# Performance work log

Hardware: AMD Instinct MI355X
Metric: run time of the kernel (lower is better)

## Reference

```python
import jax, jax.numpy as jnp
import numpy as np

B, N = 32, 4096
SA1 = (512, 0.2, 32)   # npoint, radius, nsample
SA2 = (128, 0.4, 64)
MLP1 = [3, 64, 64, 128]
MLP2 = [131, 128, 128, 256]   # 128 feats + 3 relative xyz
MLP3 = [259, 256, 512, 1024]  # 256 feats + 3 xyz (group_all)


def _mk_mlp(key, dims, prefix, d):
    for i in range(len(dims) - 1):
        key, k1 = jax.random.split(key)
        d[f"{prefix}_w{i}"] = jax.random.normal(k1, (dims[i], dims[i + 1]), jnp.float32) * (1.0 / np.sqrt(dims[i]))
        d[f"{prefix}_b{i}"] = jnp.zeros((dims[i + 1],), jnp.float32)
    return key


def setup_inputs() -> dict:
    key = jax.random.key(0)
    d = {}
    key, kx = jax.random.split(key)
    d["xyz"] = jax.random.uniform(kx, (B, N, 3), jnp.float32)  # normalized coords in [0,1)
    key = _mk_mlp(key, MLP1, "sa1", d)
    key = _mk_mlp(key, MLP2, "sa2", d)
    key = _mk_mlp(key, MLP3, "sa3", d)
    key, k1, k2 = jax.random.split(key, 3)
    d["cls_w"] = jax.random.normal(k1, (1024, 1), jnp.float32) * 0.03
    d["cls_b"] = jnp.zeros((1,), jnp.float32)
    d["reg_w"] = jax.random.normal(k2, (1024, 4), jnp.float32) * 0.03
    d["reg_b"] = jnp.zeros((4,), jnp.float32)
    return d


def fps(xyz, npoint):
    """Farthest point sampling. xyz: (B,N,3) -> idx (B,npoint) int32."""
    Bb, Nn, _ = xyz.shape

    def step(carry, _):
        dist, farthest = carry  # (B,N), (B,)
        centroid = jnp.take_along_axis(xyz, farthest[:, None, None], axis=1)  # (B,1,3)
        d = jnp.sum((xyz - centroid) ** 2, axis=-1)  # (B,N)
        dist = jnp.minimum(dist, d)
        nxt = jnp.argmax(dist, axis=-1).astype(jnp.int32)
        return (dist, nxt), farthest

    init = (jnp.full((Bb, Nn), 1e10, xyz.dtype), jnp.zeros((Bb,), jnp.int32))
    _, idx = jax.lax.scan(step, init, None, length=npoint)
    return idx.T  # (B,npoint)


def ball_query(radius, nsample, xyz, new_xyz):
    """xyz: (B,N,3), new_xyz: (B,S,3) -> idx (B,S,nsample) int32."""
    Bb, S, _ = new_xyz.shape
    Nn = xyz.shape[1]
    sqr = jnp.sum((new_xyz[:, :, None, :] - xyz[:, None, :, :]) ** 2, axis=-1)  # (B,S,N)
    idx = jnp.broadcast_to(jnp.arange(Nn, dtype=jnp.int32), (Bb, S, Nn))
    idx = jnp.where(sqr > radius * radius, Nn, idx)
    idx = jnp.sort(idx, axis=-1)[:, :, :nsample]
    first = idx[:, :, :1]
    return jnp.where(idx == Nn, first, idx)  # pad out-of-ball slots with first neighbor


def _sa(xyz, feats, npoint, radius, nsample, ws, bs):
    Bb = xyz.shape[0]
    cidx = fps(xyz, npoint)
    new_xyz = xyz[jnp.arange(Bb)[:, None], cidx]  # (B,S,3)
    gidx = ball_query(radius, nsample, xyz, new_xyz)  # (B,S,K)
    b3 = jnp.arange(Bb)[:, None, None]
    g = xyz[b3, gidx] - new_xyz[:, :, None, :]  # (B,S,K,3) relative coords
    if feats is not None:
        g = jnp.concatenate([g, feats[b3, gidx]], axis=-1)
    for w, b in zip(ws, bs):
        g = jax.nn.relu(g @ w + b)
    return new_xyz, jnp.max(g, axis=2)  # (B,S,C_out)


def _sa_all(xyz, feats, ws, bs):
    g = jnp.concatenate([xyz, feats], axis=-1)[:, None]  # (B,1,S,3+C)
    for w, b in zip(ws, bs):
        g = jax.nn.relu(g @ w + b)
    return jnp.max(g, axis=2)[:, 0]  # (B,C_out)


def reference(xyz, sa1_w0, sa1_b0, sa1_w1, sa1_b1, sa1_w2, sa1_b2,
              sa2_w0, sa2_b0, sa2_w1, sa2_b1, sa2_w2, sa2_b2,
              sa3_w0, sa3_b0, sa3_w1, sa3_b1, sa3_w2, sa3_b2,
              cls_w, cls_b, reg_w, reg_b):
    xyz1, f1 = _sa(xyz, None, SA1[0], SA1[1], SA1[2],
                   [sa1_w0, sa1_w1, sa1_w2], [sa1_b0, sa1_b1, sa1_b2])
    xyz2, f2 = _sa(xyz1, f1, SA2[0], SA2[1], SA2[2],
                   [sa2_w0, sa2_w1, sa2_w2], [sa2_b0, sa2_b1, sa2_b2])
    feat = _sa_all(xyz2, f2, [sa3_w0, sa3_w1, sa3_w2], [sa3_b0, sa3_b1, sa3_b2])  # (B,1024)
    return feat @ cls_w + cls_b, feat @ reg_w + reg_b
```

## Files before the change

### kernel.cpp

```cpp
#include <hip/hip_runtime.h>

#define DEVINL __device__ __forceinline__

typedef __attribute__((ext_vector_type(8))) short bf16x8;
typedef __attribute__((ext_vector_type(8))) unsigned short u16x8;
typedef __attribute__((ext_vector_type(4))) float f32x4;

DEVINL unsigned short f2bh(float f){
  unsigned u = __float_as_uint(f);
  return (unsigned short)((u + 0x7FFFu + ((u >> 16) & 1u)) >> 16);
}
DEVINL float bh2f(unsigned short h){ return __uint_as_float(((unsigned)h) << 16); }

DEVINL unsigned long long dpp_max_u64(unsigned long long k) {
#define DPP_STEP(ctrl)                                                        \
  {                                                                           \
    int hi = (int)(k >> 32), lo = (int)(unsigned)k;                           \
    int oh = __builtin_amdgcn_update_dpp(0, hi, ctrl, 0xF, 0xF, 1);           \
    int ol = __builtin_amdgcn_update_dpp(0, lo, ctrl, 0xF, 0xF, 1);           \
    unsigned long long ok =                                                   \
        ((unsigned long long)(unsigned)oh << 32) | (unsigned)ol;              \
    if (ok > k) k = ok;                                                       \
  }
  DPP_STEP(0x111)
  DPP_STEP(0x112)
  DPP_STEP(0x114)
  DPP_STEP(0x118)
  DPP_STEP(0x142)
  DPP_STEP(0x143)
#undef DPP_STEP
  return k;
}

template<int N, int NP, int NT>
DEVINL void fps_body(const float* __restrict__ xyz, float* __restrict__ nxyz,
                     int b, int t) {
  constexpr int PTS = N / NT;
  constexpr int NW = NT / 64;
  __shared__ float xs[N], ys[N], zs[N];
  __shared__ int farr[NP];
  __shared__ unsigned long long sk[2][(NW > 1 ? NW : 1)];
  float px[PTS], py[PTS], pz[PTS], dst[PTS];
  const float* base = xyz + (size_t)b * N * 3;
#pragma unroll
  for (int j = 0; j < PTS; ++j) {
    int i = t + j * NT;
    float x = base[i * 3 + 0], y = base[i * 3 + 1], z = base[i * 3 + 2];
    px[j] = x; py[j] = y; pz[j] = z;
    xs[i] = x; ys[i] = y; zs[i] = z;
    dst[j] = 1e10f;
  }
  if constexpr (NW > 1) __syncthreads();
  int far = 0;
  const int wv = t >> 6, ln = t & 63;
  for (int s = 0; s < NP; ++s) {
    float cx = xs[far], cy = ys[far], cz = zs[far];
    if (t == 0) farr[s] = far;
    float bv = -1.f; int bi = 0;
#pragma unroll
    for (int j = 0; j < PTS; ++j) {
      float dx = __fsub_rn(px[j], cx), dy = __fsub_rn(py[j], cy), dz = __fsub_rn(pz[j], cz);
      float d = __fadd_rn(__fadd_rn(__fmul_rn(dx, dx), __fmul_rn(dy, dy)), __fmul_rn(dz, dz));
      float nd = fminf(dst[j], d);
      dst[j] = nd;
      int i = t + j * NT;
      if (nd > bv) { bv = nd; bi = i; }
    }
    unsigned long long key =
        ((unsigned long long)__float_as_uint(bv) << 32) | (unsigned)(~bi);
    key = dpp_max_u64(key);
    if constexpr (NW == 1) {
      int rl = __builtin_amdgcn_readlane((int)(unsigned)key, 63);
      far = (int)(~(unsigned)rl);
    } else {
      const int p = s & 1;
      if (ln == 63) sk[p][wv] = key;
      __syncthreads();
      unsigned long long m = sk[p][0];
#pragma unroll
      for (int q = 1; q < NW; ++q) {
        unsigned long long qk = sk[p][q];
        if (qk > m) m = qk;
      }
      far = (int)(~(unsigned)m);
    }
  }
  if constexpr (NW > 1) __syncthreads();
  for (int s2 = t; s2 < NP; s2 += NT) {
    int fi = farr[s2];
    float* o = nxyz + ((size_t)b * NP + s2) * 3;
    o[0] = xs[fi]; o[1] = ys[fi]; o[2] = zs[fi];
  }
}

template<int N, int NS>
DEVINL void bq_body(const float* __restrict__ pts, const float* __restrict__ centers,
                    int* __restrict__ gidx, int Q, float r2, int blk, int t) {
  const int wv = t >> 6, ln = t & 63;
  const int g = blk * 4 + wv;
  const int b = g / Q, q = g % Q;
  const float* pb = pts + (size_t)b * N * 3;
  const float* c = centers + ((size_t)b * Q + q) * 3;
  const float cx = c[0], cy = c[1], cz = c[2];
  __shared__ int gbuf[4][NS];
  int taken = 0;
  for (int base = 0; base < N; base += 64) {
    if (taken >= NS) break;
    int i = base + ln;
    float dx = __fsub_rn(pb[i * 3 + 0], cx), dy = __fsub_rn(pb[i * 3 + 1], cy),
          dz = __fsub_rn(pb[i * 3 + 2], cz);
    float d = __fadd_rn(__fadd_rn(__fmul_rn(dx, dx), __fmul_rn(dy, dy)), __fmul_rn(dz, dz));
    bool in = (d <= r2);
    unsigned long long mk = __ballot(in);
    int rank = __popcll(mk & ((1ull << ln) - 1ull));
    int pos = taken + rank;
    if (in && pos < NS) gbuf[wv][pos] = i;
    taken += (int)__popcll(mk);
  }
  int total = taken < NS ? taken : NS;
  int first = gbuf[wv][0];
  int* out = gidx + ((size_t)b * Q + q) * NS;
  for (int j = ln; j < NS; j += 64) out[j] = (j < total) ? gbuf[wv][j] : first;
}

struct WPEnt { const float* W; unsigned short* hi; unsigned short* lo; int K, N, row0, beg, end; };
struct WPTab { WPEnt e[8]; };
DEVINL void wprep_body(const WPTab& tab, int idx) {
#pragma unroll
  for (int i = 0; i < 8; ++i) {
    const WPEnt& E = tab.e[i];
    if (idx >= E.beg && idx < E.end) {
      int local = idx - E.beg;
      int k = local / E.N, n = local - k * E.N;
      float v = E.W[(size_t)(E.row0 + k) * E.N + n];
      unsigned short h = f2bh(v);
      E.hi[(size_t)n * E.K + k] = h;
      E.lo[(size_t)n * E.K + k] = f2bh(v - bh2f(h));
    }
  }
}

__global__ __launch_bounds__(256) void fps1_wprep_kernel(const float* __restrict__ xyz,
                                                         float* __restrict__ nx1, WPTab tab) {
  if (blockIdx.x < 32) { fps_body<4096, 512, 256>(xyz, nx1, blockIdx.x, threadIdx.x); return; }
  wprep_body(tab, (blockIdx.x - 32) * 256 + threadIdx.x);
}

__global__ __launch_bounds__(256) void fps2_bq1_kernel(const float* __restrict__ xyz,
                                                       const float* __restrict__ nx1,
                                                       int* __restrict__ gidx1,
                                                       float* __restrict__ nx2, float r21) {
  if (blockIdx.x < 32) {
    if (threadIdx.x < 64) fps_body<512, 128, 64>(nx1, nx2, blockIdx.x, threadIdx.x);
    return;
  }
  bq_body<4096, 32>(xyz, nx1, gidx1, 512, r21, blockIdx.x - 32, threadIdx.x);
}

template<int K, int N, int CW, int AS, int WS, bool XYZC, int NTH>
DEVINL void do_layer(const unsigned short* __restrict__ Ghi, const unsigned short* __restrict__ Glo,
                     const float* __restrict__ Wxyz,
                     const float* __restrict__ A, unsigned short* __restrict__ Whi,
                     unsigned short* __restrict__ Wlo, const float* __restrict__ sxyz,
                     f32x4* acc, int t) {
  constexpr int KT = K / 32;
  constexpr int NCH = N / CW;
  constexpr int K8 = K / 8;
  constexpr int SI = (CW * K8) / NTH;
  constexpr int CT = CW / 16;
  const int l = t & 63, wv = t >> 6;

  u16x8 rh[SI], rl[SI];
#pragma unroll
  for (int s = 0; s < SI; ++s) {
    int u = t + s * NTH;
    int nn = u / K8, k8 = (u - nn * K8) * 8;
    rh[s] = *reinterpret_cast<const u16x8*>(Ghi + (size_t)nn * K + k8);
    rl[s] = *reinterpret_cast<const u16x8*>(Glo + (size_t)nn * K + k8);
  }

  bf16x8 ahi[KT], alo[KT];
  {
    const int row = wv * 16 + (l & 15);
    const float* ap = A + row * AS + (l >> 4) * 8;
#pragma unroll
    for (int kt = 0; kt < KT; ++kt) {
      float4 v0 = *reinterpret_cast<const float4*>(ap + kt * 32);
      float4 v1 = *reinterpret_cast<const float4*>(ap + kt * 32 + 4);
      float f[8] = {v0.x, v0.y, v0.z, v0.w, v1.x, v1.y, v1.z, v1.w};
      bf16x8 h, lo2;
#pragma unroll
      for (int j = 0; j < 8; ++j) {
        unsigned short hb = f2bh(f[j]);
        h[j] = (short)hb;
        lo2[j] = (short)f2bh(f[j] - bh2f(hb));
      }
      ahi[kt] = h; alo[kt] = lo2;
    }
  }
#pragma unroll
  for (int i = 0; i < N / 16; ++i) acc[i] = f32x4{0.f, 0.f, 0.f, 0.f};

#pragma unroll
  for (int c = 0; c < NCH; ++c) {
    __syncthreads();
#pragma unroll
    for (int s = 0; s < SI; ++s) {
      int u = t + s * NTH;
      int nn = u / K8, k8 = (u - nn * K8) * 8;
      *reinterpret_cast<u16x8*>(Whi + nn * WS + k8) = rh[s];
      *reinterpret_cast<u16x8*>(Wlo + nn * WS + k8) = rl[s];
    }
    if (c + 1 < NCH) {
#pragma unroll
      for (int s = 0; s < SI; ++s) {
        int u = t + s * NTH;
        int nn = u / K8, k8 = (u - nn * K8) * 8;
        rh[s] = *reinterpret_cast<const u16x8*>(Ghi + (size_t)((c + 1) * CW + nn) * K + k8);
        rl[s] = *reinterpret_cast<const u16x8*>(Glo + (size_t)((c + 1) * CW + nn) * K + k8);
      }
    }
    __syncthreads();
#pragma unroll
    for (int ct = 0; ct < CT; ++ct) {
      const unsigned short* wp = Whi + (ct * 16 + (l & 15)) * WS + (l >> 4) * 8;
      const unsigned short* wq = Wlo + (ct * 16 + (l & 15)) * WS + (l >> 4) * 8;
      f32x4 a = acc[c * CT + ct];
#pragma unroll
      for (int kt = 0; kt < KT; ++kt) {
        bf16x8 wh = *reinterpret_cast<const bf16x8*>(wp + kt * 32);
        bf16x8 wl = *reinterpret_cast<const bf16x8*>(wq + kt * 32);
        a = __builtin_amdgcn_mfma_f32_16x16x32_bf16(ahi[kt], wh, a, 0, 0, 0);
        a = __builtin_amdgcn_mfma_f32_16x16x32_bf16(alo[kt], wh, a, 0, 0, 0);
        a = __builtin_amdgcn_mfma_f32_16x16x32_bf16(ahi[kt], wl, a, 0, 0, 0);
      }
      acc[c * CT + ct] = a;
    }
  }
  if constexpr (XYZC) {
    float xr[4][3];
#pragma unroll
    for (int r = 0; r < 4; ++r) {
      int row = wv * 16 + (l >> 4) * 4 + r;
      xr[r][0] = sxyz[row * 4 + 0];
      xr[r][1] = sxyz[row * 4 + 1];
      xr[r][2] = sxyz[row * 4 + 2];
    }
#pragma unroll
    for (int gt = 0; gt < N / 16; ++gt) {
      int col = gt * 16 + (l & 15);
      float w0 = Wxyz[col], w1 = Wxyz[N + col], w2 = Wxyz[2 * N + col];
#pragma unroll
      for (int r = 0; r < 4; ++r)
        acc[gt][r] += xr[r][0] * w0 + xr[r][1] * w1 + xr[r][2] * w2;
    }
  }
}

template<int NPTS, int Q, int M, int GPB, int FD, int C1, int C2, int C3>
__global__ __launch_bounds__(512) void sa2_kernel(
    const float* __restrict__ pts, const float* __restrict__ centers,
    const int* __restrict__ gidx, const float* __restrict__ feats,
    const float* __restrict__ W0, const float* __restrict__ B0,
    const unsigned short* __restrict__ G0h, const unsigned short* __restrict__ G0l,
    const unsigned short* __restrict__ G1h, const unsigned short* __restrict__ G1l,
    const float* __restrict__ B1,
    const unsigned short* __restrict__ G2h, const unsigned short* __restrict__ G2l,
    const float* __restrict__ B2,
    float* __restrict__ fout) {
  constexpr int NTH = 512;
  constexpr int ROWS = M * GPB;
  constexpr int NWV = NTH / 64;
  static_assert(ROWS == 16 * NWV, "wave owns 16 rows");
  constexpr int MK1 = (FD > C1 ? FD : C1);
  constexpr int MAXK = (MK1 > C2 ? MK1 : C2);
  constexpr int AS = MAXK + 12;
  constexpr int WS = MAXK + 8;
  constexpr int CW = 128;
  __shared__ __align__(16) float A[ROWS * AS];
  __shared__ __align__(16) unsigned short Whi[CW * WS];
  __shared__ __align__(16) unsigned short Wlo[CW * WS];
  __shared__ float sxyz[ROWS * 4];
  __shared__ int idxs[ROWS];
  __shared__ float ctr[GPB][4];
  __shared__ float red[NWV][C3];

  const int t = threadIdx.x;
  const int blk = blockIdx.x;
  const int b = blk / (Q / GPB);
  const int q0 = (blk % (Q / GPB)) * GPB;
  const int l = t & 63, wv = t >> 6;

  if (t < GPB * 3) {
    int g = t / 3, c2 = t % 3;
    ctr[g][c2] = centers[((size_t)b * Q + q0 + g) * 3 + c2];
  }
  for (int m = t; m < ROWS; m += NTH)
    idxs[m] = gidx[((size_t)b * Q + q0 + (m / M)) * M + (m % M)];
  __syncthreads();
  const float* pb = pts + (size_t)b * NPTS * 3;
  for (int m = t; m < ROWS; m += NTH) {
    int g = m / M, i = idxs[m];
    sxyz[m * 4 + 0] = pb[i * 3 + 0] - ctr[g][0];
    sxyz[m * 4 + 1] = pb[i * 3 + 1] - ctr[g][1];
    sxyz[m * 4 + 2] = pb[i * 3 + 2] - ctr[g][2];
  }
  {
    const int m = t >> 2, co = (t & 3) * (FD / 4);
    const float* src = feats + ((size_t)b * NPTS + idxs[m]) * FD + co;
    float* dst = A + m * AS + co;
#pragma unroll
    for (int j = 0; j < FD / 4; j += 4)
      *reinterpret_cast<float4*>(dst + j) = *reinterpret_cast<const float4*>(src + j);
  }
  __syncthreads();

  f32x4 acc[C3 / 16];

  do_layer<FD, C1, CW, AS, WS, true, NTH>(G0h, G0l, W0, A, Whi, Wlo, sxyz, acc, t);
#pragma unroll
  for (int gt = 0; gt < C1 / 16; ++gt) {
    int col = gt * 16 + (l & 15);
    float bia = B0[col];
#pragma unroll
    for (int r = 0; r < 4; ++r)
      A[(wv * 16 + (l >> 4) * 4 + r) * AS + col] = fmaxf(acc[gt][r] + bia, 0.f);
  }

  do_layer<C1, C2, CW, AS, WS, false, NTH>(G1h, G1l, nullptr, A, Whi, Wlo, sxyz, acc, t);
#pragma unroll
  for (int gt = 0; gt < C2 / 16; ++gt) {
    int col = gt * 16 + (l & 15);
    float bia = B1[col];
#pragma unroll
    for (int r = 0; r < 4; ++r)
      A[(wv * 16 + (l >> 4) * 4 + r) * AS + col] = fmaxf(acc[gt][r] + bia, 0.f);
  }

  do_layer<C2, C3, CW, AS, WS, false, NTH>(G2h, G2l, nullptr, A, Whi, Wlo, sxyz, acc, t);
#pragma unroll
  for (int gt = 0; gt < C3 / 16; ++gt) {
    int col = gt * 16 + (l & 15);
    float v = fmaxf(fmaxf(acc[gt][0], acc[gt][1]), fmaxf(acc[gt][2], acc[gt][3]));
    v = fmaxf(v, __shfl_xor(v, 16, 64));
    v = fmaxf(v, __shfl_xor(v, 32, 64));
    if (l < 16) red[wv][col] = v + B2[col];
  }
  __syncthreads();
  constexpr int WPG = NWV / GPB;
  for (int u = t; u < GPB * C3; u += NTH) {
    int g = u / C3, c2 = u - g * C3;
    float v = red[g * WPG][c2];
#pragma unroll
    for (int w = 1; w < WPG; ++w) v = fmaxf(v, red[g * WPG + w][c2]);
    fout[((size_t)b * Q + q0 + g) * C3 + c2] = fmaxf(v, 0.f);
  }
}

template<int NPTS, int Q, int M, int GPB, int TPB>
DEVINL void sa1_body(const float* __restrict__ pts, const float* __restrict__ centers,
                     const int* __restrict__ gidx,
                     const float* __restrict__ W0, const float* __restrict__ B0,
                     const unsigned short* __restrict__ G1h, const unsigned short* __restrict__ G1l,
                     const float* __restrict__ B1,
                     const unsigned short* __restrict__ G2h, const unsigned short* __restrict__ G2l,
                     const float* __restrict__ B2,
                     float* __restrict__ fout, int sblk, int t) {
  static_assert(M * GPB == 64, "");
  constexpr int C1 = 64, C2 = 64, C3 = 128;
  constexpr int AS = 76;
  constexpr int WS = 72;
  constexpr int NC = C2 + C3;
  __shared__ __align__(16) float A[64 * AS];
  __shared__ __align__(16) unsigned short Wh[NC * WS];
  __shared__ __align__(16) unsigned short Wl[NC * WS];
  __shared__ float sxyz[64 * 4];
  __shared__ int idxs[64];
  __shared__ float ctr[GPB][4];
  __shared__ float red[4][C3];

  const int l = t & 63, wv = t >> 6;

  for (int u = t; u < NC * 8; u += 256) {
    int col = u >> 3, k8 = (u & 7) * 8;
    const unsigned short* sh = (col < C2) ? G1h + (size_t)col * 64 + k8
                                          : G2h + (size_t)(col - C2) * 64 + k8;
    const unsigned short* sl = (col < C2) ? G1l + (size_t)col * 64 + k8
                                          : G2l + (size_t)(col - C2) * 64 + k8;
    *reinterpret_cast<u16x8*>(Wh + col * WS + k8) = *reinterpret_cast<const u16x8*>(sh);
    *reinterpret_cast<u16x8*>(Wl + col * WS + k8) = *reinterpret_cast<const u16x8*>(sl);
  }

  for (int it = 0; it < TPB; ++it) {
    const int blk = sblk * TPB + it;
    const int b = blk / (Q / GPB);
    const int q0 = (blk % (Q / GPB)) * GPB;

    if (t < GPB * 3) {
      int g = t / 3, c2 = t % 3;
      ctr[g][c2] = centers[((size_t)b * Q + q0 + g) * 3 + c2];
    }
    for (int m = t; m < 64; m += 256)
      idxs[m] = gidx[((size_t)b * Q + q0 + (m / M)) * M + (m % M)];
    __syncthreads();
    const float* pb = pts + (size_t)b * NPTS * 3;
    for (int m = t; m < 64; m += 256) {
      int g = m / M, i = idxs[m];
      sxyz[m * 4 + 0] = pb[i * 3 + 0] - ctr[g][0];
      sxyz[m * 4 + 1] = pb[i * 3 + 1] - ctr[g][1];
      sxyz[m * 4 + 2] = pb[i * 3 + 2] - ctr[g][2];
    }
    __syncthreads();

    for (int u = t; u < 64 * C1; u += 256) {
      int m = u / C1, c2 = u - m * C1;
      float v = B0[c2] + sxyz[m * 4 + 0] * W0[0 * C1 + c2]
                       + sxyz[m * 4 + 1] * W0[1 * C1 + c2]
                       + sxyz[m * 4 + 2] * W0[2 * C1 + c2];
      A[m * AS + c2] = fmaxf(v, 0.f);
    }
    __syncthreads();

    f32x4 acc[8];
    {
      bf16x8 ah[2], al[2];
      const float* ap = A + (wv * 16 + (l & 15)) * AS + (l >> 4) * 8;
#pragma unroll
      for (int kt = 0; kt < 2; ++kt) {
        float4 v0 = *reinterpret_cast<const float4*>(ap + kt * 32);
        float4 v1 = *reinterpret_cast<const float4*>(ap + kt * 32 + 4);
        float f[8] = {v0.x, v0.y, v0.z, v0.w, v1.x, v1.y, v1.z, v1.w};
        bf16x8 h, lo2;
#pragma unroll
        for (int j = 0; j < 8; ++j) {
          unsigned short hb = f2bh(f[j]);
          h[j] = (short)hb;
          lo2[j] = (short)f2bh(f[j] - bh2f(hb));
        }
        ah[kt] = h; al[kt] = lo2;
      }
#pragma unroll
      for (int i = 0; i < 4; ++i) acc[i] = f32x4{0.f, 0.f, 0.f, 0.f};
#pragma unroll
      for (int ct = 0; ct < 4; ++ct) {
        const unsigned short* wp = Wh + (ct * 16 + (l & 15)) * WS + (l >> 4) * 8;
        const unsigned short* wq = Wl + (ct * 16 + (l & 15)) * WS + (l >> 4) * 8;
        f32x4 a = acc[ct];
#pragma unroll
        for (int kt = 0; kt < 2; ++kt) {
          bf16x8 wh = *reinterpret_cast<const bf16x8*>(wp + kt * 32);
          bf16x8 wl = *reinterpret_cast<const bf16x8*>(wq + kt * 32);
          a = __builtin_amdgcn_mfma_f32_16x16x32_bf16(ah[kt], wh, a, 0, 0, 0);
          a = __builtin_amdgcn_mfma_f32_16x16x32_bf16(al[kt], wh, a, 0, 0, 0);
          a = __builtin_amdgcn_mfma_f32_16x16x32_bf16(ah[kt], wl, a, 0, 0, 0);
        }
        acc[ct] = a;
      }
#pragma unroll
      for (int gt = 0; gt < 4; ++gt) {
        int col = gt * 16 + (l & 15);
        float bia = B1[col];
#pragma unroll
        for (int r = 0; r < 4; ++r)
          A[(wv * 16 + (l >> 4) * 4 + r) * AS + col] = fmaxf(acc[gt][r] + bia, 0.f);
      }
    }

    {
      bf16x8 ah[2], al[2];
      const float* ap = A + (wv * 16 + (l & 15)) * AS + (l >> 4) * 8;
#pragma unroll
      for (int kt = 0; kt < 2; ++kt) {
        float4 v0 = *reinterpret_cast<const float4*>(ap + kt * 32);
        float4 v1 = *reinterpret_cast<const float4*>(ap + kt * 32 + 4);
        float f[8] = {v0.x, v0.y, v0.z, v0.w, v1.x, v1.y, v1.z, v1.w};
        bf16x8 h, lo2;
#pragma unroll
        for (int j = 0; j < 8; ++j) {
          unsigned short hb = f2bh(f[j]);
          h[j] = (short)hb;
          lo2[j] = (short)f2bh(f[j] - bh2f(hb));
        }
        ah[kt] = h; al[kt] = lo2;
      }
#pragma unroll
      for (int i = 0; i < 8; ++i) acc[i] = f32x4{0.f, 0.f, 0.f, 0.f};
#pragma unroll
      for (int gt = 0; gt < 8; ++gt) {
        const unsigned short* wp = Wh + (C2 + gt * 16 + (l & 15)) * WS + (l >> 4) * 8;
        const unsigned short* wq = Wl + (C2 + gt * 16 + (l & 15)) * WS + (l >> 4) * 8;
        f32x4 a = acc[gt];
#pragma unroll
        for (int kt = 0; kt < 2; ++kt) {
          bf16x8 wh = *reinterpret_cast<const bf16x8*>(wp + kt * 32);
          bf16x8 wl = *reinterpret_cast<const bf16x8*>(wq + kt * 32);
          a = __builtin_amdgcn_mfma_f32_16x16x32_bf16(ah[kt], wh, a, 0, 0, 0);
          a = __builtin_amdgcn_mfma_f32_16x16x32_bf16(al[kt], wh, a, 0, 0, 0);
          a = __builtin_amdgcn_mfma_f32_16x16x32_bf16(ah[kt], wl, a, 0, 0, 0);
        }
        acc[gt] = a;
      }
#pragma unroll
      for (int gt = 0; gt < 8; ++gt) {
        int col = gt * 16 + (l & 15);
        float v = fmaxf(fmaxf(acc[gt][0], acc[gt][1]), fmaxf(acc[gt][2], acc[gt][3]));
        v = fmaxf(v, __shfl_xor(v, 16, 64));
        v = fmaxf(v, __shfl_xor(v, 32, 64));
        if (l < 16) red[wv][col] = v + B2[col];
      }
    }
    __syncthreads();
    constexpr int WPG = 4 / GPB;
    for (int u = t; u < GPB * C3; u += 256) {
      int g = u / C3, c2 = u - g * C3;
      float v = red[g * WPG][c2];
#pragma unroll
      for (int w = 1; w < WPG; ++w) v = fmaxf(v, red[g * WPG + w][c2]);
      fout[((size_t)b * Q + q0 + g) * C3 + c2] = fmaxf(v, 0.f);
    }
    __syncthreads();
  }
}

__global__ __launch_bounds__(256) void bq2_sa1_kernel(
    const float* __restrict__ xyz, const float* __restrict__ nx1,
    const float* __restrict__ nx2, int* __restrict__ gidx2, float r22,
    const int* __restrict__ gidx1,
    const float* __restrict__ s1w0, const float* __restrict__ s1b0,
    const unsigned short* __restrict__ g11h, const unsigned short* __restrict__ g11l,
    const float* __restrict__ s1b1,
    const unsigned short* __restrict__ g12h, const unsigned short* __restrict__ g12l,
    const float* __restrict__ s1b2, float* __restrict__ f1) {
  if (blockIdx.x < 1024) {
    bq_body<512, 64>(nx1, nx2, gidx2, 128, r22, blockIdx.x, threadIdx.x);
    return;
  }
  sa1_body<4096, 512, 32, 2, 8>(xyz, nx1, gidx1, s1w0, s1b0, g11h, g11l, s1b1,
                                g12h, g12l, s1b2, f1, blockIdx.x - 1024, threadIdx.x);
}

constexpr int AS3 = 532;
DEVINL void sa3_frags(const float* __restrict__ A, int l, int KT, bf16x8* ahi, bf16x8* alo) {
  const float* ap = A + (l & 15) * AS3 + (l >> 4) * 8;
  for (int kt = 0; kt < KT; ++kt) {
    float4 v0 = *reinterpret_cast<const float4*>(ap + kt * 32);
    float4 v1 = *reinterpret_cast<const float4*>(ap + kt * 32 + 4);
    float f[8] = {v0.x, v0.y, v0.z, v0.w, v1.x, v1.y, v1.z, v1.w};
    bf16x8 h, lo2;
#pragma unroll
    for (int j = 0; j < 8; ++j) {
      unsigned short hb = f2bh(f[j]);
      h[j] = (short)hb;
      lo2[j] = (short)f2bh(f[j] - bh2f(hb));
    }
    ahi[kt] = h; alo[kt] = lo2;
  }
}

template<int K>
DEVINL void sa3_mm64(const unsigned short* __restrict__ Gh, const unsigned short* __restrict__ Gl,
                     int ncol0, int l, const bf16x8* ahi, const bf16x8* alo, f32x4* acc4) {
  constexpr int KT = K / 32;
#pragma unroll
  for (int ct = 0; ct < 4; ++ct) {
    const unsigned short* hp = Gh + (size_t)(ncol0 + ct * 16 + (l & 15)) * K + (l >> 4) * 8;
    const unsigned short* lp = Gl + (size_t)(ncol0 + ct * 16 + (l & 15)) * K + (l >> 4) * 8;
    f32x4 a = acc4[ct];
#pragma unroll
    for (int kt = 0; kt < KT; ++kt) {
      bf16x8 wh = *reinterpret_cast<const bf16x8*>(hp + kt * 32);
      bf16x8 wl = *reinterpret_cast<const bf16x8*>(lp + kt * 32);
      a = __builtin_amdgcn_mfma_f32_16x16x32_bf16(ahi[kt], wh, a, 0, 0, 0);
      a = __builtin_amdgcn_mfma_f32_16x16x32_bf16(alo[kt], wh, a, 0, 0, 0);
      a = __builtin_amdgcn_mfma_f32_16x16x32_bf16(ahi[kt], wl, a, 0, 0, 0);
    }
    acc4[ct] = a;
  }
}

__global__ __launch_bounds__(256) void sa3f_kernel(
    const float* __restrict__ nx2, const float* __restrict__ f2,
    const float* __restrict__ W0full,
    const unsigned short* __restrict__ G0h, const unsigned short* __restrict__ G0l,
    const float* __restrict__ B0,
    const unsigned short* __restrict__ G1h, const unsigned short* __restrict__ G1l,
    const float* __restrict__ B1,
    const unsigned short* __restrict__ G2h, const unsigned short* __restrict__ G2l,
    const float* __restrict__ B2,
    float* __restrict__ partial) {
  __shared__ __align__(16) float A[16 * AS3];
  __shared__ float sxyz[16][4];
  const int t = threadIdx.x, l = t & 63, w = t >> 6;
  const int b = blockIdx.x >> 3, rb = blockIdx.x & 7;
  const int row0 = rb * 16;
  {
    int r = t >> 4, cc = (t & 15) * 16;
    const float* src = f2 + ((size_t)b * 128 + row0 + r) * 256 + cc;
    float* dstp = A + r * AS3 + cc;
#pragma unroll
    for (int j = 0; j < 16; j += 4)
      *reinterpret_cast<float4*>(dstp + j) = *reinterpret_cast<const float4*>(src + j);
    if (t < 16) {
      const float* s = nx2 + ((size_t)b * 128 + row0 + t) * 3;
      sxyz[t][0] = s[0]; sxyz[t][1] = s[1]; sxyz[t][2] = s[2];
    }
  }
  __syncthreads();

  {
    bf16x8 ah[8], al[8];
    sa3_frags(A, l, 8, ah, al);
    __syncthreads();
    f32x4 acc[4];
#pragma unroll
    for (int i = 0; i < 4; ++i) acc[i] = f32x4{0.f, 0.f, 0.f, 0.f};
    sa3_mm64<256>(G0h, G0l, w * 64, l, ah, al, acc);
    float xr[4][3];
#pragma unroll
    for (int r = 0; r < 4; ++r) {
      int row = (l >> 4) * 4 + r;
      xr[r][0] = sxyz[row][0]; xr[r][1] = sxyz[row][1]; xr[r][2] = sxyz[row][2];
    }
#pragma unroll
    for (int ct = 0; ct < 4; ++ct) {
      int col = w * 64 + ct * 16 + (l & 15);
      float w0 = W0full[col], w1 = W0full[256 + col], w2 = W0full[512 + col];
      float bia = B0[col];
#pragma unroll
      for (int r = 0; r < 4; ++r) {
        int row = (l >> 4) * 4 + r;
        float v = acc[ct][r] + xr[r][0] * w0 + xr[r][1] * w1 + xr[r][2] * w2 + bia;
        A[row * AS3 + col] = fmaxf(v, 0.f);
      }
    }
    __syncthreads();
  }

  {
    bf16x8 ah[8], al[8];
    sa3_frags(A, l, 8, ah, al);
    __syncthreads();
    f32x4 acc[8];
#pragma unroll
    for (int i = 0; i < 8; ++i) acc[i] = f32x4{0.f, 0.f, 0.f, 0.f};
    sa3_mm64<256>(G1h, G1l, w * 128, l, ah, al, acc);
    sa3_mm64<256>(G1h, G1l, w * 128 + 64, l, ah, al, acc + 4);
#pragma unroll
    for (int cc = 0; cc < 8; ++cc) {
      int col = w * 128 + cc * 16 + (l & 15);
      float bia = B1[col];
#pragma unroll
      for (int r = 0; r < 4; ++r) {
        int row = (l >> 4) * 4 + r;
        A[row * AS3 + col] = fmaxf(acc[cc][r] + bia, 0.f);
      }
    }
    __syncthreads();
  }

  {
    bf16x8 ah[16], al[16];
    sa3_frags(A, l, 16, ah, al);
    float* pout = partial + ((size_t)(b * 8 + rb)) * 1024;
#pragma unroll
    for (int sub = 0; sub < 4; ++sub) {
      f32x4 acc[4];
#pragma unroll
      for (int i = 0; i < 4; ++i) acc[i] = f32x4{0.f, 0.f, 0.f, 0.f};
      sa3_mm64<512>(G2h, G2l, w * 256 + sub * 64, l, ah, al, acc);
#pragma unroll
      for (int ct = 0; ct < 4; ++ct) {
        int col = w * 256 + sub * 64 + ct * 16 + (l & 15);
        float v = fmaxf(fmaxf(acc[ct][0], acc[ct][1]), fmaxf(acc[ct][2], acc[ct][3]));
        v = fmaxf(v, __shfl_xor(v, 16, 64));
        v = fmaxf(v, __shfl_xor(v, 32, 64));
        if (l < 16) pout[col] = v + B2[col];
      }
    }
  }
}

__global__ __launch_bounds__(256) void heads_kernel(const float* __restrict__ partial,
                                                    const float* __restrict__ cw,
                                                    const float* __restrict__ cb,
                                                    const float* __restrict__ rw,
                                                    const float* __restrict__ rb,
                                                    float* __restrict__ out) {
  const int b = blockIdx.x, t = threadIdx.x;
  const float* pb = partial + (size_t)b * 8 * 1024;
  float a0 = 0, a1 = 0, a2 = 0, a3 = 0, a4 = 0;
  for (int k = t; k < 1024; k += 256) {
    float m = pb[k];
#pragma unroll
    for (int p = 1; p < 8; ++p) m = fmaxf(m, pb[p * 1024 + k]);
    float f = fmaxf(m, 0.f);
    a0 += f * cw[k];
    const float* r = rw + (size_t)k * 4;
    a1 += f * r[0]; a2 += f * r[1]; a3 += f * r[2]; a4 += f * r[3];
  }
#pragma unroll
  for (int m = 32; m >= 1; m >>= 1) {
    a0 += __shfl_xor(a0, m, 64); a1 += __shfl_xor(a1, m, 64);
    a2 += __shfl_xor(a2, m, 64); a3 += __shfl_xor(a3, m, 64);
    a4 += __shfl_xor(a4, m, 64);
  }
  __shared__ float red[4][5];
  const int wv = t >> 6, ln = t & 63;
  if (ln == 0) { red[wv][0] = a0; red[wv][1] = a1; red[wv][2] = a2; red[wv][3] = a3; red[wv][4] = a4; }
  __syncthreads();
  if (t == 0) {
    float s0 = red[0][0] + red[1][0] + red[2][0] + red[3][0];
    float s1 = red[0][1] + red[1][1] + red[2][1] + red[3][1];
    float s2 = red[0][2] + red[1][2] + red[2][2] + red[3][2];
    float s3 = red[0][3] + red[1][3] + red[2][3] + red[3][3];
    float s4 = red[0][4] + red[1][4] + red[2][4] + red[3][4];
    out[b] = s0 + cb[0];
    out[32 + b * 4 + 0] = s1 + rb[0];
    out[32 + b * 4 + 1] = s2 + rb[1];
    out[32 + b * 4 + 2] = s3 + rb[2];
    out[32 + b * 4 + 3] = s4 + rb[3];
  }
}

extern "C" void kernel_launch(void* const* d_in, const int* in_sizes, int n_in,
                              void* d_out, int out_size, void* d_ws, size_t ws_size,
                              hipStream_t stream) {
  (void)in_sizes; (void)n_in; (void)out_size; (void)ws_size;
  const float* xyz  = (const float*)d_in[0];
  const float* s1w0 = (const float*)d_in[1];  const float* s1b0 = (const float*)d_in[2];
  const float* s1w1 = (const float*)d_in[3];  const float* s1b1 = (const float*)d_in[4];
  const float* s1w2 = (const float*)d_in[5];  const float* s1b2 = (const float*)d_in[6];
  const float* s2w0 = (const float*)d_in[7];  const float* s2b0 = (const float*)d_in[8];
  const float* s2w1 = (const float*)d_in[9];  const float* s2b1 = (const float*)d_in[10];
  const float* s2w2 = (const float*)d_in[11]; const float* s2b2 = (const float*)d_in[12];
  const float* s3w0 = (const float*)d_in[13]; const float* s3b0 = (const float*)d_in[14];
  const float* s3w1 = (const float*)d_in[15]; const float* s3b1 = (const float*)d_in[16];
  const float* s3w2 = (const float*)d_in[17]; const float* s3b2 = (const float*)d_in[18];
  const float* clsw = (const float*)d_in[19]; const float* clsb = (const float*)d_in[20];
  const float* regw = (const float*)d_in[21]; const float* regb = (const float*)d_in[22];

  char* ws = (char*)d_ws;
  float* nx1   = (float*)(ws + 0);
  int*   gidx1 = (int*)  (ws + 196608);
  float* f1    = (float*)(ws + 2293760);
  float* nx2   = (float*)(ws + 10682368);
  int*   gidx2 = (int*)  (ws + 10731520);
  float* f2    = (float*)(ws + 11780096);

  unsigned short* wt = (unsigned short*)(ws + 20168704);
  unsigned short* g11h = wt;
  unsigned short* g11l = wt + 4096;
  unsigned short* g12h = wt + 8192;
  unsigned short* g12l = wt + 16384;
  unsigned short* g20h = wt + 24576;
  unsigned short* g20l = wt + 40960;
  unsigned short* g21h = wt + 57344;
  unsigned short* g21l = wt + 73728;
  unsigned short* g22h = wt + 90112;
  unsigned short* g22l = wt + 122880;
  unsigned short* g30h = (unsigned short*)(ws + 20480000);
  unsigned short* g30l = (unsigned short*)(ws + 20611072);
  unsigned short* g31h = (unsigned short*)(ws + 20742144);
  unsigned short* g31l = (unsigned short*)(ws + 21004288);
  unsigned short* g32h = (unsigned short*)(ws + 21266432);
  unsigned short* g32l = (unsigned short*)(ws + 22315008);
  float* partial = (float*)(ws + 23363584);

  const float r21 = (float)(0.2 * 0.2);
  const float r22 = (float)(0.4 * 0.4);

  WPTab tab;
  int off = 0;
  auto set = [&](int i, const float* W, unsigned short* hi, unsigned short* lo,
                 int K, int N, int row0) {
    tab.e[i] = WPEnt{W, hi, lo, K, N, row0, off, off + K * N};
    off += K * N;
  };
  set(0, s1w1, g11h, g11l, 64, 64, 0);
  set(1, s1w2, g12h, g12l, 64, 128, 0);
  set(2, s2w0, g20h, g20l, 128, 128, 3);
  set(3, s2w1, g21h, g21l, 128, 128, 0);
  set(4, s2w2, g22h, g22l, 128, 256, 0);
  set(5, s3w0, g30h, g30l, 256, 256, 3);
  set(6, s3w1, g31h, g31l, 256, 512, 0);
  set(7, s3w2, g32h, g32l, 512, 1024, 0);
  const int wblocks = (off + 255) / 256;

  fps1_wprep_kernel<<<32 + wblocks, 256, 0, stream>>>(xyz, nx1, tab);
  fps2_bq1_kernel<<<32 + 4096, 256, 0, stream>>>(xyz, nx1, gidx1, nx2, r21);
  bq2_sa1_kernel<<<1024 + 1024, 256, 0, stream>>>(
      xyz, nx1, nx2, gidx2, r22, gidx1,
      s1w0, s1b0, g11h, g11l, s1b1, g12h, g12l, s1b2, f1);
  sa2_kernel<512, 128, 64, 2, 128, 128, 128, 256><<<2048, 512, 0, stream>>>(
      nx1, nx2, gidx2, f1, s2w0, s2b0,
      g20h, g20l, g21h, g21l, s2b1, g22h, g22l, s2b2, f2);
  sa3f_kernel<<<256, 256, 0, stream>>>(nx2, f2, s3w0, g30h, g30l, s3b0,
                                       g31h, g31l, s3b1, g32h, g32l, s3b2, partial);
  heads_kernel<<<32, 256, 0, stream>>>(partial, clsw, clsb, regw, regb, (float*)d_out);
}
```

Measured before the change: 707.3 us.

## Prefetch ball-query points, split xyz gathers per component, widen SA3 to 512 threads

The ball-query loop now loads the next 64 points into registers before handling the current chunk, and the early-exit test moves to the end of each iteration. The SA1/SA2 relative-xyz gathers spread the three coordinates across separate threads, giving the loops more parallelism. The SA3 fused kernel runs 512 threads (8 waves) per block, so each wave covers half as many output columns, which shortens per-wave MFMA chains and register pressure at the cost of more waves per block and less fragment reuse per wave.

Result: faster. 659.6 us (-6.8%).

```diff
diff --git a/kernel.cpp b/kernel.cpp
--- a/kernel.cpp
+++ b/kernel.cpp
@@ -103,12 +103,16 @@
   const float* c = centers + ((size_t)b * Q + q) * 3;
   const float cx = c[0], cy = c[1], cz = c[2];
   __shared__ int gbuf[4][NS];
+  float nx = pb[ln * 3 + 0], ny = pb[ln * 3 + 1], nz = pb[ln * 3 + 2];
   int taken = 0;
   for (int base = 0; base < N; base += 64) {
-    if (taken >= NS) break;
+    const float x = nx, y = ny, z = nz;
+    if (base + 64 < N) {
+      const float* np = pb + (size_t)(base + 64 + ln) * 3;
+      nx = np[0]; ny = np[1]; nz = np[2];
+    }
     int i = base + ln;
-    float dx = __fsub_rn(pb[i * 3 + 0], cx), dy = __fsub_rn(pb[i * 3 + 1], cy),
-          dz = __fsub_rn(pb[i * 3 + 2], cz);
+    float dx = __fsub_rn(x, cx), dy = __fsub_rn(y, cy), dz = __fsub_rn(z, cz);
     float d = __fadd_rn(__fadd_rn(__fmul_rn(dx, dx), __fmul_rn(dy, dy)), __fmul_rn(dz, dz));
     bool in = (d <= r2);
     unsigned long long mk = __ballot(in);
@@ -116,6 +120,7 @@
     int pos = taken + rank;
     if (in && pos < NS) gbuf[wv][pos] = i;
     taken += (int)__popcll(mk);
+    if (taken >= NS) break;
   }
   int total = taken < NS ? taken : NS;
   int first = gbuf[wv][0];
@@ -299,11 +304,10 @@
     idxs[m] = gidx[((size_t)b * Q + q0 + (m / M)) * M + (m % M)];
   __syncthreads();
   const float* pb = pts + (size_t)b * NPTS * 3;
-  for (int m = t; m < ROWS; m += NTH) {
+  for (int u = t; u < ROWS * 3; u += NTH) {
+    int m = u / 3, cmp = u - m * 3;
     int g = m / M, i = idxs[m];
-    sxyz[m * 4 + 0] = pb[i * 3 + 0] - ctr[g][0];
-    sxyz[m * 4 + 1] = pb[i * 3 + 1] - ctr[g][1];
-    sxyz[m * 4 + 2] = pb[i * 3 + 2] - ctr[g][2];
+    sxyz[m * 4 + cmp] = pb[i * 3 + cmp] - ctr[g][cmp];
   }
   {
     const int m = t >> 2, co = (t & 3) * (FD / 4);
@@ -404,11 +408,10 @@
       idxs[m] = gidx[((size_t)b * Q + q0 + (m / M)) * M + (m % M)];
     __syncthreads();
     const float* pb = pts + (size_t)b * NPTS * 3;
-    for (int m = t; m < 64; m += 256) {
+    for (int u = t; u < 64 * 3; u += 256) {
+      int m = u / 3, cmp = u - m * 3;
       int g = m / M, i = idxs[m];
-      sxyz[m * 4 + 0] = pb[i * 3 + 0] - ctr[g][0];
-      sxyz[m * 4 + 1] = pb[i * 3 + 1] - ctr[g][1];
-      sxyz[m * 4 + 2] = pb[i * 3 + 2] - ctr[g][2];
+      sxyz[m * 4 + cmp] = pb[i * 3 + cmp] - ctr[g][cmp];
     }
     __syncthreads();
 
@@ -557,12 +560,12 @@
   }
 }
 
-template<int K>
-DEVINL void sa3_mm64(const unsigned short* __restrict__ Gh, const unsigned short* __restrict__ Gl,
-                     int ncol0, int l, const bf16x8* ahi, const bf16x8* alo, f32x4* acc4) {
+template<int CT, int K>
+DEVINL void sa3_mmN(const unsigned short* __restrict__ Gh, const unsigned short* __restrict__ Gl,
+                    int ncol0, int l, const bf16x8* ahi, const bf16x8* alo, f32x4* acc4) {
   constexpr int KT = K / 32;
 #pragma unroll
-  for (int ct = 0; ct < 4; ++ct) {
+  for (int ct = 0; ct < CT; ++ct) {
     const unsigned short* hp = Gh + (size_t)(ncol0 + ct * 16 + (l & 15)) * K + (l >> 4) * 8;
     const unsigned short* lp = Gl + (size_t)(ncol0 + ct * 16 + (l & 15)) * K + (l >> 4) * 8;
     f32x4 a = acc4[ct];
@@ -578,7 +581,7 @@
   }
 }
 
-__global__ __launch_bounds__(256) void sa3f_kernel(
+__global__ __launch_bounds__(512) void sa3f_kernel(
     const float* __restrict__ nx2, const float* __restrict__ f2,
     const float* __restrict__ W0full,
     const unsigned short* __restrict__ G0h, const unsigned short* __restrict__ G0l,
@@ -594,11 +597,11 @@
   const int b = blockIdx.x >> 3, rb = blockIdx.x & 7;
   const int row0 = rb * 16;
   {
-    int r = t >> 4, cc = (t & 15) * 16;
+    int r = t >> 5, cc = (t & 31) * 8;
     const float* src = f2 + ((size_t)b * 128 + row0 + r) * 256 + cc;
     float* dstp = A + r * AS3 + cc;
 #pragma unroll
-    for (int j = 0; j < 16; j += 4)
+    for (int j = 0; j < 8; j += 4)
       *reinterpret_cast<float4*>(dstp + j) = *reinterpret_cast<const float4*>(src + j);
     if (t < 16) {
       const float* s = nx2 + ((size_t)b * 128 + row0 + t) * 3;
@@ -611,10 +614,10 @@
     bf16x8 ah[8], al[8];
     sa3_frags(A, l, 8, ah, al);
     __syncthreads();
-    f32x4 acc[4];
-#pragma unroll
-    for (int i = 0; i < 4; ++i) acc[i] = f32x4{0.f, 0.f, 0.f, 0.f};
-    sa3_mm64<256>(G0h, G0l, w * 64, l, ah, al, acc);
+    f32x4 acc[2];
+#pragma unroll
+    for (int i = 0; i < 2; ++i) acc[i] = f32x4{0.f, 0.f, 0.f, 0.f};
+    sa3_mmN<2, 256>(G0h, G0l, w * 32, l, ah, al, acc);
     float xr[4][3];
 #pragma unroll
     for (int r = 0; r < 4; ++r) {
@@ -622,8 +625,8 @@
       xr[r][0] = sxyz[row][0]; xr[r][1] = sxyz[row][1]; xr[r][2] = sxyz[row][2];
     }
 #pragma unroll
-    for (int ct = 0; ct < 4; ++ct) {
-      int col = w * 64 + ct * 16 + (l & 15);
+    for (int ct = 0; ct < 2; ++ct) {
+      int col = w * 32 + ct * 16 + (l & 15);
       float w0 = W0full[col], w1 = W0full[256 + col], w2 = W0full[512 + col];
       float bia = B0[col];
 #pragma unroll
@@ -640,14 +643,13 @@
     bf16x8 ah[8], al[8];
     sa3_frags(A, l, 8, ah, al);
     __syncthreads();
-    f32x4 acc[8];
-#pragma unroll
-    for (int i = 0; i < 8; ++i) acc[i] = f32x4{0.f, 0.f, 0.f, 0.f};
-    sa3_mm64<256>(G1h, G1l, w * 128, l, ah, al, acc);
-    sa3_mm64<256>(G1h, G1l, w * 128 + 64, l, ah, al, acc + 4);
-#pragma unroll
-    for (int cc = 0; cc < 8; ++cc) {
-      int col = w * 128 + cc * 16 + (l & 15);
+    f32x4 acc[4];
+#pragma unroll
+    for (int i = 0; i < 4; ++i) acc[i] = f32x4{0.f, 0.f, 0.f, 0.f};
+    sa3_mmN<4, 256>(G1h, G1l, w * 64, l, ah, al, acc);
+#pragma unroll
+    for (int cc = 0; cc < 4; ++cc) {
+      int col = w * 64 + cc * 16 + (l & 15);
       float bia = B1[col];
 #pragma unroll
       for (int r = 0; r < 4; ++r) {
@@ -663,14 +665,14 @@
     sa3_frags(A, l, 16, ah, al);
     float* pout = partial + ((size_t)(b * 8 + rb)) * 1024;
 #pragma unroll
-    for (int sub = 0; sub < 4; ++sub) {
+    for (int sub = 0; sub < 2; ++sub) {
       f32x4 acc[4];
 #pragma unroll
       for (int i = 0; i < 4; ++i) acc[i] = f32x4{0.f, 0.f, 0.f, 0.f};
-      sa3_mm64<512>(G2h, G2l, w * 256 + sub * 64, l, ah, al, acc);
+      sa3_mmN<4, 512>(G2h, G2l, w * 128 + sub * 64, l, ah, al, acc);
 #pragma unroll
       for (int ct = 0; ct < 4; ++ct) {
-        int col = w * 256 + sub * 64 + ct * 16 + (l & 15);
+        int col = w * 128 + sub * 64 + ct * 16 + (l & 15);
         float v = fmaxf(fmaxf(acc[ct][0], acc[ct][1]), fmaxf(acc[ct][2], acc[ct][3]));
         v = fmaxf(v, __shfl_xor(v, 16, 64));
         v = fmaxf(v, __shfl_xor(v, 32, 64));
@@ -794,7 +796,7 @@
   sa2_kernel<512, 128, 64, 2, 128, 128, 128, 256><<<2048, 512, 0, stream>>>(
       nx1, nx2, gidx2, f1, s2w0, s2b0,
       g20h, g20l, g21h, g21l, s2b1, g22h, g22l, s2b2, f2);
-  sa3f_kernel<<<256, 256, 0, stream>>>(nx2, f2, s3w0, g30h, g30l, s3b0,
+  sa3f_kernel<<<256, 512, 0, stream>>>(nx2, f2, s3w0, g30h, g30l, s3b0,
                                        g31h, g31l, s3b1, g32h, g32l, s3b2, partial);
   heads_kernel<<<32, 256, 0, stream>>>(partial, clsw, clsb, regw, regb, (float*)d_out);
 }
```
